# Performance work log

Measured on AMD Instinct MI355X. Metric: run time of the kernel, lower is better.

## Reference

```python
import jax, jax.numpy as jnp
import numpy as np

B, L, H = 32, 2048, 1024

def setup_inputs() -> dict:
    key = jax.random.key(0)
    ks = jax.random.split(key, 10)
    scale = 1.0 / np.sqrt(H)
    return {
        "query": jax.random.normal(ks[0], (B, 1, H), dtype=jnp.float32),
        "key": jax.random.normal(ks[1], (B, L, H), dtype=jnp.float32),
        "value": jax.random.normal(ks[2], (B, L, H), dtype=jnp.float32),
        "mask": jax.random.randint(ks[3], (B, L), 0, 2, dtype=jnp.int32),
        "Wa_w": jax.random.normal(ks[4], (H, H), dtype=jnp.float32) * scale,
        "Wa_b": jax.random.normal(ks[5], (H,), dtype=jnp.float32) * scale,
        "Ua_w": jax.random.normal(ks[6], (H, H), dtype=jnp.float32) * scale,
        "Ua_b": jax.random.normal(ks[7], (H,), dtype=jnp.float32) * scale,
        "va_w": jax.random.normal(ks[8], (1, H), dtype=jnp.float32) * scale,
        "va_b": jax.random.normal(ks[9], (1,), dtype=jnp.float32) * scale,
    }

def reference(query, key, value, mask, Wa_w, Wa_b, Ua_w, Ua_b, va_w, va_b):
    # query: [B,1,H] -> squeeze, project with Wa
    q = jnp.einsum('bh,oh->bo', query[:, 0, :], Wa_w) + Wa_b          # [B,H]
    # key: [B,L,H] projected with Ua
    k = jnp.einsum('blh,oh->blo', key, Ua_w) + Ua_b                   # [B,L,H]
    # additive score: va . tanh(Wa q + Ua h)
    s = jnp.tanh(q[:, None, :] + k)                                    # [B,L,H]
    score = jnp.einsum('blh,h->bl', s, va_w[0]) + va_b[0]             # [B,L]
    score = jnp.where(mask == 0, jnp.float32(-1e10), score)
    attn = jax.nn.softmax(score, axis=1)                               # [B,L]
    context = jnp.einsum('bl,blh->bh', attn, value)[:, None, :]       # [B,1,H]
    return context
```

## Files before the change

kernel.cpp:

```cpp
#include <hip/hip_runtime.h>
#include <hip/hip_bf16.h>


#define B_ 32
#define L_ 2048
#define H_ 1024

typedef __attribute__((ext_vector_type(8))) short bf16x8;
typedef __attribute__((ext_vector_type(16))) float f32x16;
typedef __attribute__((ext_vector_type(4))) float f32x4;

__device__ inline unsigned pk_bf16(float a, float b) {
    unsigned r;
    asm("v_cvt_pk_bf16_f32 %0, %1, %2" : "=v"(r) : "v"(a), "v"(b));
    return r;
}

__device__ inline float fast_tanh(float x) {
    float e = __expf(2.f * x);
    return 1.f - 2.f * __builtin_amdgcn_rcpf(e + 1.f);
}

__device__ inline f32x4 ntload4(const float* p) {
    return __builtin_nontemporal_load((const f32x4*)p);
}

__device__ inline int aslot(int s, int m, int lf) {
    return (((s * 2 + m) * 64) + (lf ^ ((s & 3) << 1))) * 8;
}

__global__ void prep_ua(const float* __restrict__ Ua, ushort* __restrict__ Ufrag) {
    int t = blockIdx.x * 256 + threadIdx.x;
    int lane = t & 63;
    int nb   = (t >> 6) & 31;
    int s    = t >> 11;
    int o = nb * 32 + (lane & 31);
    int h = s * 16 + (lane >> 5) * 8;
    const float* src = Ua + o * H_ + h;
    f32x4 f0 = *(const f32x4*)(src);
    f32x4 f1 = *(const f32x4*)(src + 4);
    uint4 pk;
    pk.x = pk_bf16(f0.x, f0.y);
    pk.y = pk_bf16(f0.z, f0.w);
    pk.z = pk_bf16(f1.x, f1.y);
    pk.w = pk_bf16(f1.z, f1.w);
    *(uint4*)(Ufrag + (size_t)t * 8) = pk;
}

__global__ void prep_q(const float* __restrict__ query, const float* __restrict__ Wa_w,
                       const float* __restrict__ Wa_b, const float* __restrict__ Ua_b,
                       float* __restrict__ qbuf) {
    int wid  = blockIdx.x * 4 + (threadIdx.x >> 6);
    int lane = threadIdx.x & 63;
    int b = wid >> 10, o = wid & 1023;
    const float* qrow = query + b * H_;
    const float* wrow = Wa_w + o * H_;
    float acc = 0.f;
    #pragma unroll
    for (int i = 0; i < 16; ++i) {
        int h = i * 64 + lane;
        acc += qrow[h] * wrow[h];
    }
    #pragma unroll
    for (int m = 1; m < 64; m <<= 1) acc += __shfl_xor(acc, m);
    if (lane == 0) qbuf[b * H_ + o] = acc + Wa_b[o] + Ua_b[o];
}

__launch_bounds__(512, 2)
__global__ void score_kernel(const float* __restrict__ key, const ushort* __restrict__ Ufrag,
                             const float* __restrict__ qbuf, const float* __restrict__ va_w,
                             const float* __restrict__ va_b, const int* __restrict__ mask,
                             float* __restrict__ scorebuf) {
    __shared__ ushort Alds[2][16 * 2 * 64 * 8];
    __shared__ float s_part[8][64];

    int bid = blockIdx.x;
    int b = bid >> 5, lt = bid & 31;
    int l0 = lt * 64;
    int tid = threadIdx.x;
    int w = tid >> 6, lane = tid & 63;

    int r    = tid >> 3;
    int mblk = r >> 5;
    int rr   = r & 31;
    int c0   = (tid & 7) * 8;
    const float* krow = key + ((size_t)b * L_ + (l0 + r)) * H_;

    {
        #pragma unroll
        for (int i = 0; i < 4; ++i) {
            int col = c0 + i * 64;
            f32x4 f0 = ntload4(krow + col);
            f32x4 f1 = ntload4(krow + col + 4);
            int s  = col >> 4;
            int p  = (col >> 3) & 1;
            int lf = p * 32 + rr;
            uint4 pk;
            pk.x = pk_bf16(f0.x, f0.y);
            pk.y = pk_bf16(f0.z, f0.w);
            pk.z = pk_bf16(f1.x, f1.y);
            pk.w = pk_bf16(f1.z, f1.w);
            *(uint4*)&Alds[0][aslot(s, mblk, lf)] = pk;
        }
    }

    int nb0 = w * 4;
    const ushort* Uw = Ufrag + ((size_t)nb0 * 64 + lane) * 8;

    f32x16 acc[2][4] = {};
    bf16x8 bc[4], b1[4];
    #pragma unroll
    for (int ni = 0; ni < 4; ++ni) {
        bc[ni] = *(const bf16x8*)(Uw + ni * 512);
        b1[ni] = *(const bf16x8*)(Uw + (size_t)16384 + ni * 512);
    }
    __syncthreads();

    for (int kc = 0; kc < 4; ++kc) {
        int cur = kc & 1;
        f32x4 ld[4][2];
        if (kc < 3) {
            #pragma unroll
            for (int i = 0; i < 4; ++i) {
                int col = (kc + 1) * 256 + c0 + i * 64;
                ld[i][0] = ntload4(krow + col);
                ld[i][1] = ntload4(krow + col + 4);
            }
        }
        #pragma unroll
        for (int s = 0; s < 16; ++s) {
            bf16x8 a0 = *(const bf16x8*)&Alds[cur][aslot(s, 0, lane)];
            bf16x8 a1 = *(const bf16x8*)&Alds[cur][aslot(s, 1, lane)];
            int sn = (kc * 16 + s + 2) & 63;
            bf16x8 bn[4];
            #pragma unroll
            for (int ni = 0; ni < 4; ++ni)
                bn[ni] = *(const bf16x8*)(Uw + (size_t)sn * 16384 + ni * 512);
            #pragma unroll
            for (int ni = 0; ni < 4; ++ni) {
                acc[0][ni] = __builtin_amdgcn_mfma_f32_32x32x16_bf16(a0, bc[ni], acc[0][ni], 0, 0, 0);
                acc[1][ni] = __builtin_amdgcn_mfma_f32_32x32x16_bf16(a1, bc[ni], acc[1][ni], 0, 0, 0);
            }
            #pragma unroll
            for (int ni = 0; ni < 4; ++ni) { bc[ni] = b1[ni]; b1[ni] = bn[ni]; }
        }
        if (kc < 3) {
            int nxt = cur ^ 1;
            #pragma unroll
            for (int i = 0; i < 4; ++i) {
                int col = c0 + i * 64;
                int s  = col >> 4;
                int p  = (col >> 3) & 1;
                int lf = p * 32 + rr;
                uint4 pk;
                pk.x = pk_bf16(ld[i][0].x, ld[i][0].y);
                pk.y = pk_bf16(ld[i][0].z, ld[i][0].w);
                pk.z = pk_bf16(ld[i][1].x, ld[i][1].y);
                pk.w = pk_bf16(ld[i][1].z, ld[i][1].w);
                *(uint4*)&Alds[nxt][aslot(s, mblk, lf)] = pk;
            }
            __syncthreads();
        }
    }

    float vab = va_b[0];
    #pragma unroll
    for (int mi = 0; mi < 2; ++mi) {
        float rowsum[16];
        #pragma unroll
        for (int rg = 0; rg < 16; ++rg) rowsum[rg] = 0.f;
        #pragma unroll
        for (int ni = 0; ni < 4; ++ni) {
            int col = w * 128 + ni * 32 + (lane & 31);
            float qv  = qbuf[b * H_ + col];
            float vav = va_w[col];
            #pragma unroll
            for (int rg = 0; rg < 16; ++rg)
                rowsum[rg] += vav * fast_tanh(qv + acc[mi][ni][rg]);
        }
        #pragma unroll
        for (int rg = 0; rg < 16; ++rg) {
            float v = rowsum[rg];
            v += __shfl_xor(v, 1);  v += __shfl_xor(v, 2);  v += __shfl_xor(v, 4);
            v += __shfl_xor(v, 8);  v += __shfl_xor(v, 16);
            if ((lane & 31) == 0) {
                int row = mi * 32 + (rg & 3) + 8 * (rg >> 2) + 4 * (lane >> 5);
                s_part[w][row] = v;
            }
        }
    }
    __syncthreads();
    if (tid < 64) {
        float s = 0.f;
        #pragma unroll
        for (int ww = 0; ww < 8; ++ww) s += s_part[ww][tid];
        int l = l0 + tid;
        int m = mask[b * L_ + l];
        scorebuf[b * L_ + l] = (m == 0) ? -1e10f : (s + vab);
    }
}

__global__ void softmax_kernel(const float* __restrict__ scorebuf, float* __restrict__ attn) {
    __shared__ float red[16];
    int b = blockIdx.x;
    int tid = threadIdx.x;
    float v[8];
    float mx = -3e38f;
    #pragma unroll
    for (int i = 0; i < 8; ++i) {
        v[i] = scorebuf[b * L_ + tid + i * 256];
        mx = fmaxf(mx, v[i]);
    }
    #pragma unroll
    for (int m = 1; m < 64; m <<= 1) mx = fmaxf(mx, __shfl_xor(mx, m));
    if ((tid & 63) == 0) red[tid >> 6] = mx;
    __syncthreads();
    mx = fmaxf(fmaxf(red[0], red[1]), fmaxf(red[2], red[3]));
    float sum = 0.f;
    #pragma unroll
    for (int i = 0; i < 8; ++i) { v[i] = __expf(v[i] - mx); sum += v[i]; }
    #pragma unroll
    for (int m = 1; m < 64; m <<= 1) sum += __shfl_xor(sum, m);
    if ((tid & 63) == 0) red[8 + (tid >> 6)] = sum;
    __syncthreads();
    sum = red[8] + red[9] + red[10] + red[11];
    float inv = 1.f / sum;
    #pragma unroll
    for (int i = 0; i < 8; ++i) attn[b * L_ + tid + i * 256] = v[i] * inv;
}

__global__ void context_kernel(const float* __restrict__ attn, const float* __restrict__ value,
                               float* __restrict__ partial) {
    int bid = blockIdx.x;
    int b = bid >> 4, ch = bid & 15;
    int l0 = ch * 128;
    int tid = threadIdx.x;
    f32x4 acc = {0.f, 0.f, 0.f, 0.f};
    const float* vbase = value + ((size_t)b * L_ + l0) * H_ + tid * 4;
    const float* arow  = attn + b * L_ + l0;
    for (int l = 0; l < 128; ++l) {
        float a = arow[l];
        f32x4 vv = *(const f32x4*)(vbase + (size_t)l * H_);
        acc.x += a * vv.x; acc.y += a * vv.y; acc.z += a * vv.z; acc.w += a * vv.w;
    }
    *(f32x4*)(partial + (size_t)bid * H_ + tid * 4) = acc;
}

__global__ void reduce_kernel(const float* __restrict__ partial, float* __restrict__ out) {
    int t = blockIdx.x * 256 + threadIdx.x;
    int b = t >> 10, h = t & 1023;
    float s = 0.f;
    #pragma unroll
    for (int c = 0; c < 16; ++c) s += partial[(size_t)(b * 16 + c) * H_ + h];
    out[t] = s;
}

extern "C" void kernel_launch(void* const* d_in, const int* in_sizes, int n_in,
                              void* d_out, int out_size, void* d_ws, size_t ws_size,
                              hipStream_t stream) {
    const float* query = (const float*)d_in[0];
    const float* key   = (const float*)d_in[1];
    const float* value = (const float*)d_in[2];
    const int*   mask  = (const int*)d_in[3];
    const float* Wa_w  = (const float*)d_in[4];
    const float* Wa_b  = (const float*)d_in[5];
    const float* Ua_w  = (const float*)d_in[6];
    const float* Ua_b  = (const float*)d_in[7];
    const float* va_w  = (const float*)d_in[8];
    const float* va_b  = (const float*)d_in[9];
    float* out = (float*)d_out;

    char* ws = (char*)d_ws;
    ushort* Ufrag    = (ushort*)ws;
    float*  qbuf     = (float*)(ws + (2u << 20));
    float*  scorebuf = (float*)(ws + (2u << 20) + (128u << 10));
    float*  attnb    = (float*)(ws + (2u << 20) + (384u << 10));
    float*  partial  = (float*)(ws + (2u << 20) + (640u << 10));

    hipLaunchKernelGGL(prep_ua,        dim3(512),  dim3(256), 0, stream, Ua_w, Ufrag);
    hipLaunchKernelGGL(prep_q,         dim3(8192), dim3(256), 0, stream, query, Wa_w, Wa_b, Ua_b, qbuf);
    hipLaunchKernelGGL(score_kernel,   dim3(1024), dim3(512), 0, stream, key, Ufrag, qbuf, va_w, va_b, mask, scorebuf);
    hipLaunchKernelGGL(softmax_kernel, dim3(32),   dim3(256), 0, stream, scorebuf, attnb);
    hipLaunchKernelGGL(context_kernel, dim3(512),  dim3(256), 0, stream, attnb, value, partial);
    hipLaunchKernelGGL(reduce_kernel,  dim3(128),  dim3(256), 0, stream, partial, out);
}
```

Before: 252.9 us.

## Retile score GEMM to 128 rows by half the output columns, split score reduction

The score kernel now processes 128 key rows per block while covering only half of the H output columns, so each warp does 4x2 MFMA tiles instead of 2x4. The two column halves write separate partial scores, and the softmax kernel sums them and applies the bias and mask. The key tile load is split into two half-chunks, one issued mid-loop, and Ua fragments are prefetched three steps ahead in a 4-deep ring. The aim is to halve repeated Ua fragment loads per key row and to spread global load latency. The cost is double the LDS footprint per block, extra partial-score traffic, and each key row being loaded by two blocks.

```diff
diff --git a/kernel.cpp b/kernel.cpp
--- a/kernel.cpp
+++ b/kernel.cpp
@@ -26,7 +26,7 @@
 }
 
 __device__ inline int aslot(int s, int m, int lf) {
-    return (((s * 2 + m) * 64) + (lf ^ ((s & 3) << 1))) * 8;
+    return (((s * 4 + m) * 64) + (lf ^ ((s & 3) << 1))) * 8;
 }
 
 __global__ void prep_ua(const float* __restrict__ Ua, ushort* __restrict__ Ufrag) {
@@ -69,27 +69,28 @@
 __launch_bounds__(512, 2)
 __global__ void score_kernel(const float* __restrict__ key, const ushort* __restrict__ Ufrag,
                              const float* __restrict__ qbuf, const float* __restrict__ va_w,
-                             const float* __restrict__ va_b, const int* __restrict__ mask,
-                             float* __restrict__ scorebuf) {
-    __shared__ ushort Alds[2][16 * 2 * 64 * 8];
-    __shared__ float s_part[8][64];
+                             float* __restrict__ pscore) {
+    __shared__ ushort Alds[2][16 * 4 * 64 * 8];
+    __shared__ float s_part[8][128];
 
     int bid = blockIdx.x;
-    int b = bid >> 5, lt = bid & 31;
-    int l0 = lt * 64;
+    int oh = bid & 1;
+    int lt = (bid >> 1) & 15;
+    int b  = bid >> 5;
+    int l0 = lt * 128;
     int tid = threadIdx.x;
     int w = tid >> 6, lane = tid & 63;
 
-    int r    = tid >> 3;
+    int r    = tid >> 2;
     int mblk = r >> 5;
     int rr   = r & 31;
-    int c0   = (tid & 7) * 8;
+    int c0   = (tid & 3) * 8;
     const float* krow = key + ((size_t)b * L_ + (l0 + r)) * H_;
 
     {
         #pragma unroll
-        for (int i = 0; i < 4; ++i) {
-            int col = c0 + i * 64;
+        for (int j = 0; j < 8; ++j) {
+            int col = c0 + j * 32;
             f32x4 f0 = ntload4(krow + col);
             f32x4 f1 = ntload4(krow + col + 4);
             int s  = col >> 4;
@@ -104,74 +105,94 @@
         }
     }
 
-    int nb0 = w * 4;
+    int nb0 = oh * 16 + w * 2;
     const ushort* Uw = Ufrag + ((size_t)nb0 * 64 + lane) * 8;
 
-    f32x16 acc[2][4] = {};
-    bf16x8 bc[4], b1[4];
-    #pragma unroll
-    for (int ni = 0; ni < 4; ++ni) {
-        bc[ni] = *(const bf16x8*)(Uw + ni * 512);
-        b1[ni] = *(const bf16x8*)(Uw + (size_t)16384 + ni * 512);
-    }
+    f32x16 acc[4][2] = {};
+    bf16x8 bb[4][2];
+    #pragma unroll
+    for (int k = 0; k < 3; ++k)
+        #pragma unroll
+        for (int ni = 0; ni < 2; ++ni)
+            bb[k][ni] = *(const bf16x8*)(Uw + (size_t)k * 16384 + ni * 512);
     __syncthreads();
 
     for (int kc = 0; kc < 4; ++kc) {
         int cur = kc & 1;
-        f32x4 ld[4][2];
+        int nxt = cur ^ 1;
+        f32x4 ld[8];
         if (kc < 3) {
             #pragma unroll
-            for (int i = 0; i < 4; ++i) {
-                int col = (kc + 1) * 256 + c0 + i * 64;
-                ld[i][0] = ntload4(krow + col);
-                ld[i][1] = ntload4(krow + col + 4);
+            for (int j = 0; j < 4; ++j) {
+                int col = (kc + 1) * 256 + c0 + j * 32;
+                ld[2*j]   = ntload4(krow + col);
+                ld[2*j+1] = ntload4(krow + col + 4);
             }
         }
         #pragma unroll
         for (int s = 0; s < 16; ++s) {
             bf16x8 a0 = *(const bf16x8*)&Alds[cur][aslot(s, 0, lane)];
             bf16x8 a1 = *(const bf16x8*)&Alds[cur][aslot(s, 1, lane)];
-            int sn = (kc * 16 + s + 2) & 63;
-            bf16x8 bn[4];
+            bf16x8 a2 = *(const bf16x8*)&Alds[cur][aslot(s, 2, lane)];
+            bf16x8 a3 = *(const bf16x8*)&Alds[cur][aslot(s, 3, lane)];
+            int gp = (kc * 16 + s + 3) & 63;
             #pragma unroll
-            for (int ni = 0; ni < 4; ++ni)
-                bn[ni] = *(const bf16x8*)(Uw + (size_t)sn * 16384 + ni * 512);
+            for (int ni = 0; ni < 2; ++ni)
+                bb[(s + 3) & 3][ni] = *(const bf16x8*)(Uw + (size_t)gp * 16384 + ni * 512);
+            acc[0][0] = __builtin_amdgcn_mfma_f32_32x32x16_bf16(a0, bb[s & 3][0], acc[0][0], 0, 0, 0);
+            acc[1][0] = __builtin_amdgcn_mfma_f32_32x32x16_bf16(a1, bb[s & 3][0], acc[1][0], 0, 0, 0);
+            acc[2][0] = __builtin_amdgcn_mfma_f32_32x32x16_bf16(a2, bb[s & 3][0], acc[2][0], 0, 0, 0);
+            acc[3][0] = __builtin_amdgcn_mfma_f32_32x32x16_bf16(a3, bb[s & 3][0], acc[3][0], 0, 0, 0);
+            acc[0][1] = __builtin_amdgcn_mfma_f32_32x32x16_bf16(a0, bb[s & 3][1], acc[0][1], 0, 0, 0);
+            acc[1][1] = __builtin_amdgcn_mfma_f32_32x32x16_bf16(a1, bb[s & 3][1], acc[1][1], 0, 0, 0);
+            acc[2][1] = __builtin_amdgcn_mfma_f32_32x32x16_bf16(a2, bb[s & 3][1], acc[2][1], 0, 0, 0);
+            acc[3][1] = __builtin_amdgcn_mfma_f32_32x32x16_bf16(a3, bb[s & 3][1], acc[3][1], 0, 0, 0);
+            if (s == 7 && kc < 3) {
+                #pragma unroll
+                for (int j = 0; j < 4; ++j) {
+                    int col = c0 + j * 32;
+                    int ss = col >> 4, p = (col >> 3) & 1;
+                    int lf = p * 32 + rr;
+                    uint4 pk;
+                    pk.x = pk_bf16(ld[2*j].x,   ld[2*j].y);
+                    pk.y = pk_bf16(ld[2*j].z,   ld[2*j].w);
+                    pk.z = pk_bf16(ld[2*j+1].x, ld[2*j+1].y);
+                    pk.w = pk_bf16(ld[2*j+1].z, ld[2*j+1].w);
+                    *(uint4*)&Alds[nxt][aslot(ss, mblk, lf)] = pk;
+                }
+                #pragma unroll
+                for (int j = 0; j < 4; ++j) {
+                    int col = (kc + 1) * 256 + 128 + c0 + j * 32;
+                    ld[2*j]   = ntload4(krow + col);
+                    ld[2*j+1] = ntload4(krow + col + 4);
+                }
+            }
+        }
+        if (kc < 3) {
             #pragma unroll
-            for (int ni = 0; ni < 4; ++ni) {
-                acc[0][ni] = __builtin_amdgcn_mfma_f32_32x32x16_bf16(a0, bc[ni], acc[0][ni], 0, 0, 0);
-                acc[1][ni] = __builtin_amdgcn_mfma_f32_32x32x16_bf16(a1, bc[ni], acc[1][ni], 0, 0, 0);
-            }
-            #pragma unroll
-            for (int ni = 0; ni < 4; ++ni) { bc[ni] = b1[ni]; b1[ni] = bn[ni]; }
-        }
-        if (kc < 3) {
-            int nxt = cur ^ 1;
-            #pragma unroll
-            for (int i = 0; i < 4; ++i) {
-                int col = c0 + i * 64;
-                int s  = col >> 4;
-                int p  = (col >> 3) & 1;
+            for (int j = 0; j < 4; ++j) {
+                int col = 128 + c0 + j * 32;
+                int ss = col >> 4, p = (col >> 3) & 1;
                 int lf = p * 32 + rr;
                 uint4 pk;
-                pk.x = pk_bf16(ld[i][0].x, ld[i][0].y);
-                pk.y = pk_bf16(ld[i][0].z, ld[i][0].w);
-                pk.z = pk_bf16(ld[i][1].x, ld[i][1].y);
-                pk.w = pk_bf16(ld[i][1].z, ld[i][1].w);
-                *(uint4*)&Alds[nxt][aslot(s, mblk, lf)] = pk;
+                pk.x = pk_bf16(ld[2*j].x,   ld[2*j].y);
+                pk.y = pk_bf16(ld[2*j].z,   ld[2*j].w);
+                pk.z = pk_bf16(ld[2*j+1].x, ld[2*j+1].y);
+                pk.w = pk_bf16(ld[2*j+1].z, ld[2*j+1].w);
+                *(uint4*)&Alds[nxt][aslot(ss, mblk, lf)] = pk;
             }
             __syncthreads();
         }
     }
 
-    float vab = va_b[0];
-    #pragma unroll
-    for (int mi = 0; mi < 2; ++mi) {
+    #pragma unroll
+    for (int mi = 0; mi < 4; ++mi) {
         float rowsum[16];
         #pragma unroll
         for (int rg = 0; rg < 16; ++rg) rowsum[rg] = 0.f;
         #pragma unroll
-        for (int ni = 0; ni < 4; ++ni) {
-            int col = w * 128 + ni * 32 + (lane & 31);
+        for (int ni = 0; ni < 2; ++ni) {
+            int col = (nb0 + ni) * 32 + (lane & 31);
             float qv  = qbuf[b * H_ + col];
             float vav = va_w[col];
             #pragma unroll
@@ -190,25 +211,28 @@
         }
     }
     __syncthreads();
-    if (tid < 64) {
+    if (tid < 128) {
         float s = 0.f;
         #pragma unroll
         for (int ww = 0; ww < 8; ++ww) s += s_part[ww][tid];
-        int l = l0 + tid;
-        int m = mask[b * L_ + l];
-        scorebuf[b * L_ + l] = (m == 0) ? -1e10f : (s + vab);
-    }
-}
-
-__global__ void softmax_kernel(const float* __restrict__ scorebuf, float* __restrict__ attn) {
+        pscore[((size_t)oh * B_ + b) * L_ + l0 + tid] = s;
+    }
+}
+
+__global__ void softmax_kernel(const float* __restrict__ pscore, const float* __restrict__ va_b,
+                               const int* __restrict__ mask, float* __restrict__ attn) {
     __shared__ float red[16];
     int b = blockIdx.x;
     int tid = threadIdx.x;
+    float vab = va_b[0];
     float v[8];
     float mx = -3e38f;
     #pragma unroll
     for (int i = 0; i < 8; ++i) {
-        v[i] = scorebuf[b * L_ + tid + i * 256];
+        int l = tid + i * 256;
+        float s = pscore[b * L_ + l] + pscore[(size_t)B_ * L_ + b * L_ + l] + vab;
+        int m = mask[b * L_ + l];
+        v[i] = (m == 0) ? -1e10f : s;
         mx = fmaxf(mx, v[i]);
     }
     #pragma unroll
@@ -273,14 +297,14 @@
     char* ws = (char*)d_ws;
     ushort* Ufrag    = (ushort*)ws;
     float*  qbuf     = (float*)(ws + (2u << 20));
-    float*  scorebuf = (float*)(ws + (2u << 20) + (128u << 10));
-    float*  attnb    = (float*)(ws + (2u << 20) + (384u << 10));
-    float*  partial  = (float*)(ws + (2u << 20) + (640u << 10));
+    float*  pscore   = (float*)(ws + (2u << 20) + (128u << 10));
+    float*  attnb    = (float*)(ws + (2u << 20) + (640u << 10));
+    float*  partial  = (float*)(ws + (2u << 20) + (896u << 10));
 
     hipLaunchKernelGGL(prep_ua,        dim3(512),  dim3(256), 0, stream, Ua_w, Ufrag);
     hipLaunchKernelGGL(prep_q,         dim3(8192), dim3(256), 0, stream, query, Wa_w, Wa_b, Ua_b, qbuf);
-    hipLaunchKernelGGL(score_kernel,   dim3(1024), dim3(512), 0, stream, key, Ufrag, qbuf, va_w, va_b, mask, scorebuf);
-    hipLaunchKernelGGL(softmax_kernel, dim3(32),   dim3(256), 0, stream, scorebuf, attnb);
+    hipLaunchKernelGGL(score_kernel,   dim3(1024), dim3(512), 0, stream, key, Ufrag, qbuf, va_w, pscore);
+    hipLaunchKernelGGL(softmax_kernel, dim3(32),   dim3(256), 0, stream, pscore, va_b, mask, attnb);
     hipLaunchKernelGGL(context_kernel, dim3(512),  dim3(256), 0, stream, attnb, value, partial);
     hipLaunchKernelGGL(reduce_kernel,  dim3(128),  dim3(256), 0, stream, partial, out);
 }
```

Result: slower. 291.4 us (+15.2%).

## Split score kernel across 16 waves with narrower per-wave N tiles

Applied to the files above, without the earlier changes.

Doubles score_kernel blocks to 1024 threads, with each wave now owning 2 N-tiles (64 output columns) instead of 4. This halves accumulator registers per wave and aims at more waves in flight to hide key-load and Ufrag-load latency. Each thread now loads 16 contiguous floats per K-chunk, and the LDS swizzle changes to xor with s&7. The risks are more Ufrag traffic, since each A tile is reused by fewer MFMAs per wave, and a larger cross-wave reduction at the end.

```diff
diff --git a/kernel.cpp b/kernel.cpp
--- a/kernel.cpp
+++ b/kernel.cpp
@@ -26,7 +26,7 @@
 }
 
 __device__ inline int aslot(int s, int m, int lf) {
-    return (((s * 2 + m) * 64) + (lf ^ ((s & 3) << 1))) * 8;
+    return (((s * 2 + m) * 64) + (lf ^ (s & 7))) * 8;
 }
 
 __global__ void prep_ua(const float* __restrict__ Ua, ushort* __restrict__ Ufrag) {
@@ -66,13 +66,13 @@
     if (lane == 0) qbuf[b * H_ + o] = acc + Wa_b[o] + Ua_b[o];
 }
 
-__launch_bounds__(512, 2)
+__launch_bounds__(1024, 4)
 __global__ void score_kernel(const float* __restrict__ key, const ushort* __restrict__ Ufrag,
                              const float* __restrict__ qbuf, const float* __restrict__ va_w,
                              const float* __restrict__ va_b, const int* __restrict__ mask,
                              float* __restrict__ scorebuf) {
-    __shared__ ushort Alds[2][16 * 2 * 64 * 8];
-    __shared__ float s_part[8][64];
+    __shared__ ushort Alds[2][16384];
+    __shared__ float s_part[16][64];
 
     int bid = blockIdx.x;
     int b = bid >> 5, lt = bid & 31;
@@ -80,98 +80,87 @@
     int tid = threadIdx.x;
     int w = tid >> 6, lane = tid & 63;
 
-    int r    = tid >> 3;
+    int r    = tid >> 4;
+    int c0s  = tid & 15;
+    int c0   = c0s * 16;
     int mblk = r >> 5;
     int rr   = r & 31;
-    int c0   = (tid & 7) * 8;
     const float* krow = key + ((size_t)b * L_ + (l0 + r)) * H_;
 
-    {
-        #pragma unroll
-        for (int i = 0; i < 4; ++i) {
-            int col = c0 + i * 64;
-            f32x4 f0 = ntload4(krow + col);
-            f32x4 f1 = ntload4(krow + col + 4);
-            int s  = col >> 4;
-            int p  = (col >> 3) & 1;
-            int lf = p * 32 + rr;
-            uint4 pk;
-            pk.x = pk_bf16(f0.x, f0.y);
-            pk.y = pk_bf16(f0.z, f0.w);
-            pk.z = pk_bf16(f1.x, f1.y);
-            pk.w = pk_bf16(f1.z, f1.w);
-            *(uint4*)&Alds[0][aslot(s, mblk, lf)] = pk;
-        }
-    }
-
-    int nb0 = w * 4;
+    int nb0 = w * 2;
     const ushort* Uw = Ufrag + ((size_t)nb0 * 64 + lane) * 8;
 
-    f32x16 acc[2][4] = {};
-    bf16x8 bc[4], b1[4];
-    #pragma unroll
-    for (int ni = 0; ni < 4; ++ni) {
+    f32x4 ld[4];
+    #pragma unroll
+    for (int i = 0; i < 4; ++i) ld[i] = ntload4(krow + c0 + 4 * i);
+    bf16x8 bc[2], b1[2];
+    #pragma unroll
+    for (int ni = 0; ni < 2; ++ni) {
         bc[ni] = *(const bf16x8*)(Uw + ni * 512);
         b1[ni] = *(const bf16x8*)(Uw + (size_t)16384 + ni * 512);
     }
-    __syncthreads();
+    {
+        uint4 pk0, pk1;
+        pk0.x = pk_bf16(ld[0].x, ld[0].y);
+        pk0.y = pk_bf16(ld[0].z, ld[0].w);
+        pk0.z = pk_bf16(ld[1].x, ld[1].y);
+        pk0.w = pk_bf16(ld[1].z, ld[1].w);
+        pk1.x = pk_bf16(ld[2].x, ld[2].y);
+        pk1.y = pk_bf16(ld[2].z, ld[2].w);
+        pk1.z = pk_bf16(ld[3].x, ld[3].y);
+        pk1.w = pk_bf16(ld[3].z, ld[3].w);
+        *(uint4*)&Alds[0][aslot(c0s, mblk, rr)]      = pk0;
+        *(uint4*)&Alds[0][aslot(c0s, mblk, 32 + rr)] = pk1;
+    }
+    __syncthreads();
+
+    f32x16 acc[2][2] = {};
 
     for (int kc = 0; kc < 4; ++kc) {
         int cur = kc & 1;
-        f32x4 ld[4][2];
         if (kc < 3) {
             #pragma unroll
-            for (int i = 0; i < 4; ++i) {
-                int col = (kc + 1) * 256 + c0 + i * 64;
-                ld[i][0] = ntload4(krow + col);
-                ld[i][1] = ntload4(krow + col + 4);
-            }
-        }
-        #pragma unroll
+            for (int i = 0; i < 4; ++i)
+                ld[i] = ntload4(krow + (kc + 1) * 256 + c0 + 4 * i);
+        }
+        #pragma unroll 4
         for (int s = 0; s < 16; ++s) {
             bf16x8 a0 = *(const bf16x8*)&Alds[cur][aslot(s, 0, lane)];
             bf16x8 a1 = *(const bf16x8*)&Alds[cur][aslot(s, 1, lane)];
-            int sn = (kc * 16 + s + 2) & 63;
-            bf16x8 bn[4];
-            #pragma unroll
-            for (int ni = 0; ni < 4; ++ni)
-                bn[ni] = *(const bf16x8*)(Uw + (size_t)sn * 16384 + ni * 512);
-            #pragma unroll
-            for (int ni = 0; ni < 4; ++ni) {
-                acc[0][ni] = __builtin_amdgcn_mfma_f32_32x32x16_bf16(a0, bc[ni], acc[0][ni], 0, 0, 0);
-                acc[1][ni] = __builtin_amdgcn_mfma_f32_32x32x16_bf16(a1, bc[ni], acc[1][ni], 0, 0, 0);
-            }
-            #pragma unroll
-            for (int ni = 0; ni < 4; ++ni) { bc[ni] = b1[ni]; b1[ni] = bn[ni]; }
+            int gp = (kc * 16 + s + 2) & 63;
+            bf16x8 bn0 = *(const bf16x8*)(Uw + (size_t)gp * 16384);
+            bf16x8 bn1 = *(const bf16x8*)(Uw + (size_t)gp * 16384 + 512);
+            acc[0][0] = __builtin_amdgcn_mfma_f32_32x32x16_bf16(a0, bc[0], acc[0][0], 0, 0, 0);
+            acc[1][0] = __builtin_amdgcn_mfma_f32_32x32x16_bf16(a1, bc[0], acc[1][0], 0, 0, 0);
+            acc[0][1] = __builtin_amdgcn_mfma_f32_32x32x16_bf16(a0, bc[1], acc[0][1], 0, 0, 0);
+            acc[1][1] = __builtin_amdgcn_mfma_f32_32x32x16_bf16(a1, bc[1], acc[1][1], 0, 0, 0);
+            bc[0] = b1[0]; bc[1] = b1[1];
+            b1[0] = bn0;   b1[1] = bn1;
         }
         if (kc < 3) {
-            int nxt = cur ^ 1;
-            #pragma unroll
-            for (int i = 0; i < 4; ++i) {
-                int col = c0 + i * 64;
-                int s  = col >> 4;
-                int p  = (col >> 3) & 1;
-                int lf = p * 32 + rr;
-                uint4 pk;
-                pk.x = pk_bf16(ld[i][0].x, ld[i][0].y);
-                pk.y = pk_bf16(ld[i][0].z, ld[i][0].w);
-                pk.z = pk_bf16(ld[i][1].x, ld[i][1].y);
-                pk.w = pk_bf16(ld[i][1].z, ld[i][1].w);
-                *(uint4*)&Alds[nxt][aslot(s, mblk, lf)] = pk;
-            }
+            uint4 pk0, pk1;
+            pk0.x = pk_bf16(ld[0].x, ld[0].y);
+            pk0.y = pk_bf16(ld[0].z, ld[0].w);
+            pk0.z = pk_bf16(ld[1].x, ld[1].y);
+            pk0.w = pk_bf16(ld[1].z, ld[1].w);
+            pk1.x = pk_bf16(ld[2].x, ld[2].y);
+            pk1.y = pk_bf16(ld[2].z, ld[2].w);
+            pk1.z = pk_bf16(ld[3].x, ld[3].y);
+            pk1.w = pk_bf16(ld[3].z, ld[3].w);
+            *(uint4*)&Alds[cur ^ 1][aslot(c0s, mblk, rr)]      = pk0;
+            *(uint4*)&Alds[cur ^ 1][aslot(c0s, mblk, 32 + rr)] = pk1;
             __syncthreads();
         }
     }
 
-    float vab = va_b[0];
     #pragma unroll
     for (int mi = 0; mi < 2; ++mi) {
         float rowsum[16];
         #pragma unroll
         for (int rg = 0; rg < 16; ++rg) rowsum[rg] = 0.f;
         #pragma unroll
-        for (int ni = 0; ni < 4; ++ni) {
-            int col = w * 128 + ni * 32 + (lane & 31);
+        for (int ni = 0; ni < 2; ++ni) {
+            int col = w * 64 + ni * 32 + (lane & 31);
             float qv  = qbuf[b * H_ + col];
             float vav = va_w[col];
             #pragma unroll
@@ -193,10 +182,10 @@
     if (tid < 64) {
         float s = 0.f;
         #pragma unroll
-        for (int ww = 0; ww < 8; ++ww) s += s_part[ww][tid];
+        for (int ww = 0; ww < 16; ++ww) s += s_part[ww][tid];
         int l = l0 + tid;
         int m = mask[b * L_ + l];
-        scorebuf[b * L_ + l] = (m == 0) ? -1e10f : (s + vab);
+        scorebuf[b * L_ + l] = (m == 0) ? -1e10f : (s + va_b[0]);
     }
 }
 
@@ -277,10 +266,10 @@
     float*  attnb    = (float*)(ws + (2u << 20) + (384u << 10));
     float*  partial  = (float*)(ws + (2u << 20) + (640u << 10));
 
-    hipLaunchKernelGGL(prep_ua,        dim3(512),  dim3(256), 0, stream, Ua_w, Ufrag);
-    hipLaunchKernelGGL(prep_q,         dim3(8192), dim3(256), 0, stream, query, Wa_w, Wa_b, Ua_b, qbuf);
-    hipLaunchKernelGGL(score_kernel,   dim3(1024), dim3(512), 0, stream, key, Ufrag, qbuf, va_w, va_b, mask, scorebuf);
-    hipLaunchKernelGGL(softmax_kernel, dim3(32),   dim3(256), 0, stream, scorebuf, attnb);
-    hipLaunchKernelGGL(context_kernel, dim3(512),  dim3(256), 0, stream, attnb, value, partial);
-    hipLaunchKernelGGL(reduce_kernel,  dim3(128),  dim3(256), 0, stream, partial, out);
-}
+    hipLaunchKernelGGL(prep_ua,        dim3(512),  dim3(256),  0, stream, Ua_w, Ufrag);
+    hipLaunchKernelGGL(prep_q,         dim3(8192), dim3(256),  0, stream, query, Wa_w, Wa_b, Ua_b, qbuf);
+    hipLaunchKernelGGL(score_kernel,   dim3(1024), dim3(1024), 0, stream, key, Ufrag, qbuf, va_w, va_b, mask, scorebuf);
+    hipLaunchKernelGGL(softmax_kernel, dim3(32),   dim3(256),  0, stream, scorebuf, attnb);
+    hipLaunchKernelGGL(context_kernel, dim3(512),  dim3(256),  0, stream, attnb, value, partial);
+    hipLaunchKernelGGL(reduce_kernel,  dim3(128),  dim3(256),  0, stream, partial, out);
+}
```

Result: slower. 275.4 us (+8.9%).
